# Optimization experiments

Hardware: AMD Instinct MI355X
Metric: run time of the kernel (lower is better)

The kernel has to match this reference:

```python
import jax, jax.numpy as jnp
import numpy as np

G = 4
EPS = 1e-5

def group_norm(x, gamma, beta):
    B, C, D, H, W = x.shape
    xg = x.reshape(B, G, C // G, D, H, W)
    mu = xg.mean(axis=(2, 3, 4, 5), keepdims=True)
    var = xg.var(axis=(2, 3, 4, 5), keepdims=True)
    xn = ((xg - mu) * jax.lax.rsqrt(var + EPS)).reshape(B, C, D, H, W)
    return xn * gamma[None, :, None, None, None] + beta[None, :, None, None, None]

def conv3d(x, w, b):
    y = jax.lax.conv_general_dilated(x, w, (1, 1, 1), [(1, 1), (1, 1), (1, 1)],
                                     dimension_numbers=('NCDHW', 'OIDHW', 'NCDHW'))
    return y + b[None, :, None, None, None]

def deform_conv_hw(x, offset, w, b):
    # x: [B,C,D,H,W]; offset: [B, 2*27, D,H,W] -> per-tap (dh, dw); depth taps are rigid.
    B, C, D, H, W = x.shape
    off = offset.reshape(B, 27, 2, D, H, W)
    xp = jnp.pad(x, ((0, 0), (0, 0), (1, 1), (0, 0), (0, 0)))  # zero-pad depth only
    hh = jnp.arange(H, dtype=x.dtype)[None, None, :, None]
    ww = jnp.arange(W, dtype=x.dtype)[None, None, None, :]
    bi = jnp.arange(B)[:, None, None, None]
    di = jnp.arange(D)[None, :, None, None]
    out = jnp.zeros((B, w.shape[0], D, H, W), x.dtype)
    tap = 0
    for i in range(3):
        x_d = xp[:, :, i:i + D]  # depth-shifted view [B,C,D,H,W]
        for j in range(3):
            for k in range(3):
                hp = hh + (j - 1) + off[:, tap, 0]  # [B,D,H,W] fractional h position
                wp = ww + (k - 1) + off[:, tap, 1]
                h0 = jnp.floor(hp); w0 = jnp.floor(wp)
                h0i = h0.astype(jnp.int32); w0i = w0.astype(jnp.int32)
                lh = hp - h0; lw = wp - w0
                def gather(hi, wi):
                    m = ((hi >= 0) & (hi < H) & (wi >= 0) & (wi < W)).astype(x.dtype)
                    g = x_d[bi, :, di, jnp.clip(hi, 0, H - 1), jnp.clip(wi, 0, W - 1)]  # [B,D,H,W,C]
                    return g, m
                g00, m00 = gather(h0i, w0i)
                g01, m01 = gather(h0i, w0i + 1)
                g10, m10 = gather(h0i + 1, w0i)
                g11, m11 = gather(h0i + 1, w0i + 1)
                val = (((1 - lh) * (1 - lw) * m00)[..., None] * g00
                       + ((1 - lh) * lw * m01)[..., None] * g01
                       + (lh * (1 - lw) * m10)[..., None] * g10
                       + (lh * lw * m11)[..., None] * g11)
                out = out + jnp.einsum('bdhwc,oc->bodhw', val, w[:, :, i, j, k])
                tap += 1
    return out + b[None, :, None, None, None]

def setup_inputs():
    key = jax.random.key(0)
    ks = jax.random.split(key, 8)
    B, C, D, H, W = 1, 32, 24, 96, 96
    x = jax.random.normal(ks[0], (B, C, D, H, W), jnp.float32)
    g1 = jnp.ones((C,), jnp.float32); be1 = jnp.zeros((C,), jnp.float32)
    g2 = jnp.ones((C,), jnp.float32); be2 = jnp.zeros((C,), jnp.float32)
    ow1 = jax.random.normal(ks[1], (54, C, 3, 3, 3), jnp.float32) * 0.02
    ob1 = jnp.zeros((54,), jnp.float32)
    dw1 = jax.random.normal(ks[2], (C, C, 3, 3, 3), jnp.float32) * 0.05
    db1 = jnp.zeros((C,), jnp.float32)
    ow2 = jax.random.normal(ks[3], (54, C, 3, 3, 3), jnp.float32) * 0.02
    ob2 = jnp.zeros((54,), jnp.float32)
    dw2 = jax.random.normal(ks[4], (C, C, 3, 3, 3), jnp.float32) * 0.05
    db2 = jnp.zeros((C,), jnp.float32)
    return {"x": x, "g1": g1, "be1": be1, "g2": g2, "be2": be2,
            "ow1": ow1, "ob1": ob1, "dw1": dw1, "db1": db1,
            "ow2": ow2, "ob2": ob2, "dw2": dw2, "db2": db2}

def reference(x, g1, be1, g2, be2, ow1, ob1, dw1, db1, ow2, ob2, dw2, db2):
    h = jax.nn.relu(group_norm(x, g1, be1))
    h = deform_conv_hw(h, conv3d(h, ow1, ob1), dw1, db1)
    h = jax.nn.relu(group_norm(h, g2, be2))
    h = deform_conv_hw(h, conv3d(h, ow2, ob2), dw2, db2)
    return h + x
```

## Files before the change

### kernel.cpp

```cpp
#include <hip/hip_runtime.h>
#include <hip/hip_fp16.h>

#define CC   32
#define DD   24
#define HH   96
#define WW   96
#define HWC  (HH*WW)
#define DHW  (DD*HH*WW)
#define NG   4
#define CPG  (CC/NG)
#define OC1  54
#define GN_EPS 1e-5f

#define NBLK_F (DHW/128)
#define CHUNK_F (NBLK_F/8)
#define NBLK_G (DHW/256)
#define CHUNK_G (NBLK_G/8)

typedef float  f32x4 __attribute__((ext_vector_type(4)));
typedef _Float16 f16x8 __attribute__((ext_vector_type(8)));
typedef unsigned int u32x4 __attribute__((ext_vector_type(4)));

union F16Frag { f16x8 v; __half2 h2[4]; };

__device__ __forceinline__ int swz(int bid, int chunk) {
    return (bid % 8) * chunk + (bid / 8);
}

__global__ void pack_w(const float* __restrict__ src, _Float16* __restrict__ dst,
                       int O, int NT, int n) {
    int idx = blockIdx.x * 256 + threadIdx.x;
    if (idx >= n) return;
    int e    = idx & 7;
    int lane = (idx >> 3) & 63;
    int nt   = (idx >> 9) % NT;
    int tap  = (idx >> 9) / NT;
    int o = nt * 16 + (lane & 15);
    int c = (lane >> 4) * 8 + e;
    float v = (o < O) ? src[(o * CC + c) * 27 + tap] : 0.f;
    dst[idx] = (_Float16)v;
}

__global__ void gn_stats(const float* __restrict__ x, float* __restrict__ stats) {
    const int g = blockIdx.x >> 5;
    const int s = blockIdx.x & 31;
    const float4* base = (const float4*)(x + (size_t)g * CPG * DHW);
    const int n4 = CPG * DHW / 4;
    float s1 = 0.f, s2 = 0.f;
    for (int idx = s * 256 + threadIdx.x; idx < n4; idx += 32 * 256) {
        float4 v = base[idx];
        s1 += v.x + v.y + v.z + v.w;
        s2 += v.x * v.x + v.y * v.y + v.z * v.z + v.w * v.w;
    }
    for (int off = 32; off > 0; off >>= 1) {
        s1 += __shfl_down(s1, off);
        s2 += __shfl_down(s2, off);
    }
    __shared__ float ls1[4], ls2[4];
    int wid = threadIdx.x >> 6;
    if ((threadIdx.x & 63) == 0) { ls1[wid] = s1; ls2[wid] = s2; }
    __syncthreads();
    if (threadIdx.x == 0) {
        float a = 0.f, b = 0.f;
        for (int i = 0; i < 4; i++) { a += ls1[i]; b += ls2[i]; }
        atomicAdd(&stats[g * 2 + 0], a);
        atomicAdd(&stats[g * 2 + 1], b);
    }
}

__global__ void gn_apply_T(const float* __restrict__ x, const float* __restrict__ stats,
                           const float* __restrict__ gamma, const float* __restrict__ beta,
                           __half* __restrict__ yT) {
    const int p = swz(blockIdx.x, CHUNK_G) * 256 + threadIdx.x;
    const float invN = 1.0f / (float)(CPG * DHW);
    float mean[NG], rstd[NG];
#pragma unroll
    for (int g = 0; g < NG; g++) {
        mean[g] = stats[2 * g] * invN;
        float var = stats[2 * g + 1] * invN - mean[g] * mean[g];
        rstd[g] = rsqrtf(var + GN_EPS);
    }
    float vals[CC];
#pragma unroll
    for (int c = 0; c < CC; c++) {
        const int g = c >> 3;
        const float ga = gamma[c] * rstd[g];
        const float be = beta[c] - mean[g] * ga;
        vals[c] = fmaxf(0.f, x[(size_t)c * DHW + p] * ga + be);
    }
    union { __half2 h2[16]; u32x4 q[4]; } u;
#pragma unroll
    for (int c = 0; c < 16; c++) u.h2[c] = __floats2half2_rn(vals[2 * c], vals[2 * c + 1]);
    u32x4* dst = (u32x4*)(yT + (size_t)p * CC);
#pragma unroll
    for (int q = 0; q < 4; q++) dst[q] = u.q[q];
}

__global__ __launch_bounds__(128, 3) void fused_conv(const __half* __restrict__ xT,
                                                     const _Float16* __restrict__ wBo,
                                                     const float* __restrict__ ob,
                                                     const _Float16* __restrict__ wBd,
                                                     const float* __restrict__ db,
                                                     const float* __restrict__ resid,
                                                     float* __restrict__ outp) {
    __shared__ __align__(16) char lds_raw[CC * 132 * 4];
    __half* offs_lds = (__half*)lds_raw;
    float*  out_lds  = (float*)lds_raw;

    const int tid  = threadIdx.x;
    const int lane = tid & 63;
    const int wave = tid >> 6;
    const int p0   = swz(blockIdx.x, CHUNK_F) * 128;
    const int pw   = p0 + wave * 64;
    const int d    = pw / HWC;
    const int rem  = pw % HWC;
    const int mrow = lane & 15;
    const int kg   = lane >> 4;
    const int wbase2 = wave * (27 * 64 * 2);

    int hq[4], wq[4];
#pragma unroll
    for (int m = 0; m < 4; m++) {
        int rr = rem + m * 16 + mrow;
        hq[m] = rr / WW; wq[m] = rr % WW;
    }

    f32x4 aco[4][4];
#pragma unroll
    for (int m = 0; m < 4; m++)
#pragma unroll
        for (int n = 0; n < 4; n++) aco[m][n] = (f32x4){0.f, 0.f, 0.f, 0.f};

    const f16x8* wbo8 = (const f16x8*)wBo;

#pragma unroll 1
    for (int i = 0; i < 3; i++) {
        const int dd = d + i - 1;
        if ((unsigned)dd >= DD) continue;
        const __half* xd = xT + (size_t)dd * HWC * CC;
#pragma unroll 3
        for (int jk = 0; jk < 9; jk++) {
            const int j = jk / 3, k = jk % 3, tap = i * 9 + jk;
            const f16x8 b0 = wbo8[(tap * 4 + 0) * 64 + lane];
            const f16x8 b1 = wbo8[(tap * 4 + 1) * 64 + lane];
            const f16x8 b2 = wbo8[(tap * 4 + 2) * 64 + lane];
            const f16x8 b3 = wbo8[(tap * 4 + 3) * 64 + lane];
            f16x8 a[4];
#pragma unroll
            for (int m = 0; m < 4; m++) {
                const int hh = hq[m] + j - 1;
                const int ww = wq[m] + k - 1;
                a[m] = (f16x8){0, 0, 0, 0, 0, 0, 0, 0};
                if ((unsigned)hh < HH && (unsigned)ww < WW)
                    a[m] = *(const f16x8*)(xd + (size_t)(hh * WW + ww) * CC + kg * 8);
            }
#pragma unroll
            for (int m = 0; m < 4; m++) {
                aco[m][0] = __builtin_amdgcn_mfma_f32_16x16x32_f16(a[m], b0, aco[m][0], 0, 0, 0);
                aco[m][1] = __builtin_amdgcn_mfma_f32_16x16x32_f16(a[m], b1, aco[m][1], 0, 0, 0);
                aco[m][2] = __builtin_amdgcn_mfma_f32_16x16x32_f16(a[m], b2, aco[m][2], 0, 0, 0);
                aco[m][3] = __builtin_amdgcn_mfma_f32_16x16x32_f16(a[m], b3, aco[m][3], 0, 0, 0);
            }
        }
    }

    float bo[4];
#pragma unroll
    for (int nt = 0; nt < 4; nt++) {
        const int o = nt * 16 + mrow;
        bo[nt] = (o < OC1) ? ob[o] : 0.f;
    }
#pragma unroll
    for (int m = 0; m < 4; m++) {
#pragma unroll
        for (int nt = 0; nt < 4; nt++) {
            const int o = nt * 16 + mrow;
            if (o < OC1) {
                const int tap = o >> 1, par = o & 1;
#pragma unroll
                for (int r = 0; r < 4; r++) {
                    const int pt = m * 16 + kg * 4 + r;
                    offs_lds[wbase2 + tap * 128 + pt * 2 + par] =
                        __float2half(aco[m][nt][r] + bo[nt]);
                }
            }
        }
    }
    __syncthreads();

    f32x4 acd[4][2];
#pragma unroll
    for (int m = 0; m < 4; m++) {
        acd[m][0] = (f32x4){0.f, 0.f, 0.f, 0.f};
        acd[m][1] = (f32x4){0.f, 0.f, 0.f, 0.f};
    }

    const f16x8* wbd8 = (const f16x8*)wBd;

#pragma unroll 1
    for (int i = 0; i < 3; i++) {
        const int dd = d + i - 1;
        if ((unsigned)dd >= DD) continue;
        const __half* xd = xT + (size_t)dd * HWC * CC;
        unsigned int offn[4];
#pragma unroll
        for (int m = 0; m < 4; m++)
            offn[m] = *(const unsigned int*)&offs_lds[wbase2 + (i * 9) * 128 + (m * 16 + mrow) * 2];
#pragma unroll 1
        for (int jk = 0; jk < 9; jk++) {
            const int j = jk / 3, k = jk % 3, tap = i * 9 + jk;
            const f16x8 b0 = wbd8[(tap * 2 + 0) * 64 + lane];
            const f16x8 b1 = wbd8[(tap * 2 + 1) * 64 + lane];
            unsigned int offc[4];
#pragma unroll
            for (int m = 0; m < 4; m++) offc[m] = offn[m];
            if (jk < 8) {
#pragma unroll
                for (int m = 0; m < 4; m++)
                    offn[m] = *(const unsigned int*)&offs_lds[wbase2 + (tap + 1) * 128 + (m * 16 + mrow) * 2];
            }
            int i00[4], i01[4], i10[4], i11[4];
            float c00[4], c01[4], c10[4], c11[4];
#pragma unroll
            for (int m = 0; m < 4; m++) {
                const __half2 o2 = *(__half2*)&offc[m];
                const float oh = __half2float(__low2half(o2));
                const float ov = __half2float(__high2half(o2));
                const float hp  = (float)(hq[m] + j - 1) + oh;
                const float wpf = (float)(wq[m] + k - 1) + ov;
                const float h0f = floorf(hp), w0f = floorf(wpf);
                const int h0 = (int)h0f, w0 = (int)w0f;
                const float lh = hp - h0f, lw = wpf - w0f;
                const bool hv0 = (h0 >= 0) && (h0 < HH);
                const bool hv1 = (h0 >= -1) && (h0 < HH - 1);
                const bool wv0 = (w0 >= 0) && (w0 < WW);
                const bool wv1 = (w0 >= -1) && (w0 < WW - 1);
                c00[m] = (hv0 && wv0) ? (1.f - lh) * (1.f - lw) : 0.f;
                c01[m] = (hv0 && wv1) ? (1.f - lh) * lw : 0.f;
                c10[m] = (hv1 && wv0) ? lh * (1.f - lw) : 0.f;
                c11[m] = (hv1 && wv1) ? lh * lw : 0.f;
                const int h0c = min(max(h0, 0), HH - 1);
                const int h1c = min(max(h0 + 1, 0), HH - 1);
                const int w0c = min(max(w0, 0), WW - 1);
                const int w1c = min(max(w0 + 1, 0), WW - 1);
                i00[m] = h0c * WW + w0c;
                i01[m] = h0c * WW + w1c;
                i10[m] = h1c * WW + w0c;
                i11[m] = h1c * WW + w1c;
            }
#pragma unroll
            for (int m = 0; m < 4; m++) {
                F16Frag a00, a01, a10, a11, A;
                a00.v = *(const f16x8*)(xd + (size_t)i00[m] * CC + kg * 8);
                a01.v = *(const f16x8*)(xd + (size_t)i01[m] * CC + kg * 8);
                a10.v = *(const f16x8*)(xd + (size_t)i10[m] * CC + kg * 8);
                a11.v = *(const f16x8*)(xd + (size_t)i11[m] * CC + kg * 8);
                const __half2 C00 = __float2half2_rn(c00[m]);
                const __half2 C01 = __float2half2_rn(c01[m]);
                const __half2 C10 = __float2half2_rn(c10[m]);
                const __half2 C11 = __float2half2_rn(c11[m]);
#pragma unroll
                for (int r = 0; r < 4; r++) {
                    __half2 t = __hmul2(C00, a00.h2[r]);
                    t = __hfma2(C01, a01.h2[r], t);
                    t = __hfma2(C10, a10.h2[r], t);
                    t = __hfma2(C11, a11.h2[r], t);
                    A.h2[r] = t;
                }
                acd[m][0] = __builtin_amdgcn_mfma_f32_16x16x32_f16(A.v, b0, acd[m][0], 0, 0, 0);
                acd[m][1] = __builtin_amdgcn_mfma_f32_16x16x32_f16(A.v, b1, acd[m][1], 0, 0, 0);
            }
        }
    }
    __syncthreads();

#pragma unroll
    for (int m = 0; m < 4; m++)
#pragma unroll
        for (int nt = 0; nt < 2; nt++) {
            const int o = nt * 16 + mrow;
            *(f32x4*)&out_lds[o * 132 + wave * 64 + m * 16 + kg * 4] = acd[m][nt];
        }
    __syncthreads();
    if (resid) {
#pragma unroll 1
        for (int o = 0; o < CC; o++) {
            float v = out_lds[o * 132 + tid] + db[o] + resid[(size_t)o * DHW + p0 + tid];
            outp[(size_t)o * DHW + p0 + tid] = v;
        }
    } else {
#pragma unroll 1
        for (int o = 0; o < CC; o++)
            outp[(size_t)o * DHW + p0 + tid] = out_lds[o * 132 + tid] + db[o];
    }
}

extern "C" void kernel_launch(void* const* d_in, const int* in_sizes, int n_in,
                              void* d_out, int out_size, void* d_ws, size_t ws_size,
                              hipStream_t stream) {
    const float* x   = (const float*)d_in[0];
    const float* g1  = (const float*)d_in[1];
    const float* be1 = (const float*)d_in[2];
    const float* g2  = (const float*)d_in[3];
    const float* be2 = (const float*)d_in[4];
    const float* ow1 = (const float*)d_in[5];
    const float* ob1 = (const float*)d_in[6];
    const float* dw1 = (const float*)d_in[7];
    const float* db1 = (const float*)d_in[8];
    const float* ow2 = (const float*)d_in[9];
    const float* ob2 = (const float*)d_in[10];
    const float* dw2 = (const float*)d_in[11];
    const float* db2 = (const float*)d_in[12];
    float* out = (float*)d_out;
    float* ws  = (float*)d_ws;

    float*    stats = ws;
    _Float16* wBo1  = (_Float16*)(ws + 256);
    _Float16* wBd1  = (_Float16*)(ws + 27904);
    _Float16* wBo2  = (_Float16*)(ws + 41728);
    _Float16* wBd2  = (_Float16*)(ws + 69376);
    __half*   hT    = (__half*)(ws + 83200);

    (void)hipMemsetAsync(stats, 0, 16 * sizeof(float), stream);
    pack_w<<<(27 * 4 * 512 + 255) / 256, 256, 0, stream>>>(ow1, wBo1, 54, 4, 27 * 4 * 512);
    pack_w<<<(27 * 2 * 512 + 255) / 256, 256, 0, stream>>>(dw1, wBd1, 32, 2, 27 * 2 * 512);
    pack_w<<<(27 * 4 * 512 + 255) / 256, 256, 0, stream>>>(ow2, wBo2, 54, 4, 27 * 4 * 512);
    pack_w<<<(27 * 2 * 512 + 255) / 256, 256, 0, stream>>>(dw2, wBd2, 32, 2, 27 * 2 * 512);

    gn_stats<<<NG * 32, 256, 0, stream>>>(x, stats + 0);
    gn_apply_T<<<NBLK_G, 256, 0, stream>>>(x, stats + 0, g1, be1, hT);
    fused_conv<<<NBLK_F, 128, 0, stream>>>(hT, wBo1, ob1, wBd1, db1, nullptr, out);

    gn_stats<<<NG * 32, 256, 0, stream>>>(out, stats + 8);
    gn_apply_T<<<NBLK_G, 256, 0, stream>>>(out, stats + 8, g2, be2, hT);
    fused_conv<<<NBLK_F, 128, 0, stream>>>(hT, wBo2, ob2, wBd2, db2, x, out);
}
```

Measured before the change: 368.2 us.

## Stage halo input rows into LDS for the offset convolution

For each depth tap, the block cooperatively loads four padded input rows (the block's rows plus a one-row halo) into shared memory, using a padded channel stride. The nine h/w taps then read their MFMA A fragments from LDS instead of issuing repeated global loads. This trades redundant global and cache traffic for two barriers per depth slice and a larger LDS footprint, which may limit occupancy.

```diff
diff --git a/kernel.cpp b/kernel.cpp
--- a/kernel.cpp
+++ b/kernel.cpp
@@ -16,6 +16,9 @@
 #define CHUNK_F (NBLK_F/8)
 #define NBLK_G (DHW/256)
 #define CHUNK_G (NBLK_G/8)
+
+#define XS_STRIDE 40
+#define XS_PTS    (4*WW)
 
 typedef float  f32x4 __attribute__((ext_vector_type(4)));
 typedef _Float16 f16x8 __attribute__((ext_vector_type(8)));
@@ -103,7 +106,8 @@
                                                      const float* __restrict__ db,
                                                      const float* __restrict__ resid,
                                                      float* __restrict__ outp) {
-    __shared__ __align__(16) char lds_raw[CC * 132 * 4];
+    __shared__ __align__(16) char lds_raw[XS_PTS * XS_STRIDE * 2];
+    __half* xs       = (__half*)lds_raw;
     __half* offs_lds = (__half*)lds_raw;
     float*  out_lds  = (float*)lds_raw;
 
@@ -112,7 +116,8 @@
     const int wave = tid >> 6;
     const int p0   = swz(blockIdx.x, CHUNK_F) * 128;
     const int pw   = p0 + wave * 64;
-    const int d    = pw / HWC;
+    const int d    = p0 / HWC;
+    const int r0   = (p0 % HWC) / WW;
     const int rem  = pw % HWC;
     const int mrow = lane & 15;
     const int kg   = lane >> 4;
@@ -137,7 +142,23 @@
     for (int i = 0; i < 3; i++) {
         const int dd = d + i - 1;
         if ((unsigned)dd >= DD) continue;
-        const __half* xd = xT + (size_t)dd * HWC * CC;
+        const __half* xsrc = xT + (size_t)dd * HWC * CC;
+
+        __syncthreads();
+#pragma unroll
+        for (int rd = 0; rd < 12; rd++) {
+            const int fi  = rd * 128 + tid;
+            const int pt  = fi >> 2;
+            const int q   = fi & 3;
+            const int row = r0 - 1 + (pt / WW);
+            const int wc  = pt % WW;
+            f16x8 v = {0, 0, 0, 0, 0, 0, 0, 0};
+            if ((unsigned)row < HH)
+                v = *(const f16x8*)(xsrc + ((size_t)row * WW + wc) * CC + q * 8);
+            *(f16x8*)(xs + pt * XS_STRIDE + q * 8) = v;
+        }
+        __syncthreads();
+
 #pragma unroll 3
         for (int jk = 0; jk < 9; jk++) {
             const int j = jk / 3, k = jk % 3, tap = i * 9 + jk;
@@ -148,11 +169,11 @@
             f16x8 a[4];
 #pragma unroll
             for (int m = 0; m < 4; m++) {
-                const int hh = hq[m] + j - 1;
+                const int lr = hq[m] + j - r0;
                 const int ww = wq[m] + k - 1;
                 a[m] = (f16x8){0, 0, 0, 0, 0, 0, 0, 0};
-                if ((unsigned)hh < HH && (unsigned)ww < WW)
-                    a[m] = *(const f16x8*)(xd + (size_t)(hh * WW + ww) * CC + kg * 8);
+                if ((unsigned)ww < WW)
+                    a[m] = *(const f16x8*)(xs + (size_t)(lr * WW + ww) * XS_STRIDE + kg * 8);
             }
 #pragma unroll
             for (int m = 0; m < 4; m++) {
@@ -163,6 +184,7 @@
             }
         }
     }
+    __syncthreads();
 
     float bo[4];
 #pragma unroll
```

After: 389.7 us. +5.8%, slower.

## Fuse second GroupNorm statistics into first conv epilogue and merge weight packing

Applied to the files above, without the earlier changes.

The first fused_conv now accumulates per-group sum and sum-of-squares of its output in the store loop, reduces them across each wave with shuffles, and adds them to global stats with atomics. This removes the separate gn_stats pass that re-read the whole intermediate tensor. The four pack_w launches and the memset are merged into one pack_all kernel to cut launch overhead. In exchange, fp32 atomic accumulation order becomes nondeterministic, and the conv epilogue carries extra register pressure and about 2k atomics per group.

```diff
diff --git a/kernel.cpp b/kernel.cpp
--- a/kernel.cpp
+++ b/kernel.cpp
@@ -27,18 +27,29 @@
     return (bid % 8) * chunk + (bid / 8);
 }
 
-__global__ void pack_w(const float* __restrict__ src, _Float16* __restrict__ dst,
-                       int O, int NT, int n) {
+__global__ void pack_all(const float* __restrict__ ow1, const float* __restrict__ dw1,
+                         const float* __restrict__ ow2, const float* __restrict__ dw2,
+                         _Float16* __restrict__ wBo1, _Float16* __restrict__ wBd1,
+                         _Float16* __restrict__ wBo2, _Float16* __restrict__ wBd2,
+                         float* __restrict__ stats) {
     int idx = blockIdx.x * 256 + threadIdx.x;
-    if (idx >= n) return;
-    int e    = idx & 7;
-    int lane = (idx >> 3) & 63;
-    int nt   = (idx >> 9) % NT;
-    int tap  = (idx >> 9) / NT;
+    if (blockIdx.x == 0 && threadIdx.x < 16) stats[threadIdx.x] = 0.f;
+    const int NO = 27 * 4 * 512;
+    const int ND = 27 * 2 * 512;
+    const float* src; _Float16* dst; int O, NT, rel;
+    if (idx < NO)                       { src = ow1; dst = wBo1; O = 54; NT = 4; rel = idx; }
+    else if (idx < NO + ND)             { src = dw1; dst = wBd1; O = 32; NT = 2; rel = idx - NO; }
+    else if (idx < 2 * NO + ND)         { src = ow2; dst = wBo2; O = 54; NT = 4; rel = idx - NO - ND; }
+    else if (idx < 2 * NO + 2 * ND)     { src = dw2; dst = wBd2; O = 32; NT = 2; rel = idx - 2 * NO - ND; }
+    else return;
+    int e    = rel & 7;
+    int lane = (rel >> 3) & 63;
+    int nt   = (rel >> 9) % NT;
+    int tap  = (rel >> 9) / NT;
     int o = nt * 16 + (lane & 15);
     int c = (lane >> 4) * 8 + e;
     float v = (o < O) ? src[(o * CC + c) * 27 + tap] : 0.f;
-    dst[idx] = (_Float16)v;
+    dst[rel] = (_Float16)v;
 }
 
 __global__ void gn_stats(const float* __restrict__ x, float* __restrict__ stats) {
@@ -102,7 +113,8 @@
                                                      const _Float16* __restrict__ wBd,
                                                      const float* __restrict__ db,
                                                      const float* __restrict__ resid,
-                                                     float* __restrict__ outp) {
+                                                     float* __restrict__ outp,
+                                                     float* __restrict__ stats_out) {
     __shared__ __align__(16) char lds_raw[CC * 132 * 4];
     __half* offs_lds = (__half*)lds_raw;
     float*  out_lds  = (float*)lds_raw;
@@ -289,9 +301,31 @@
             outp[(size_t)o * DHW + p0 + tid] = v;
         }
     } else {
-#pragma unroll 1
-        for (int o = 0; o < CC; o++)
-            outp[(size_t)o * DHW + p0 + tid] = out_lds[o * 132 + tid] + db[o];
+        float s1l[NG] = {0.f, 0.f, 0.f, 0.f};
+        float s2l[NG] = {0.f, 0.f, 0.f, 0.f};
+#pragma unroll 1
+        for (int o = 0; o < CC; o++) {
+            float v = out_lds[o * 132 + tid] + db[o];
+            outp[(size_t)o * DHW + p0 + tid] = v;
+            s1l[o >> 3] += v;
+            s2l[o >> 3] += v * v;
+        }
+        if (stats_out) {
+            for (int off = 32; off > 0; off >>= 1) {
+#pragma unroll
+                for (int g = 0; g < NG; g++) {
+                    s1l[g] += __shfl_down(s1l[g], off);
+                    s2l[g] += __shfl_down(s2l[g], off);
+                }
+            }
+            if (lane == 0) {
+#pragma unroll
+                for (int g = 0; g < NG; g++) {
+                    atomicAdd(&stats_out[2 * g + 0], s1l[g]);
+                    atomicAdd(&stats_out[2 * g + 1], s2l[g]);
+                }
+            }
+        }
     }
 }
 
@@ -321,17 +355,13 @@
     _Float16* wBd2  = (_Float16*)(ws + 69376);
     __half*   hT    = (__half*)(ws + 83200);
 
-    (void)hipMemsetAsync(stats, 0, 16 * sizeof(float), stream);
-    pack_w<<<(27 * 4 * 512 + 255) / 256, 256, 0, stream>>>(ow1, wBo1, 54, 4, 27 * 4 * 512);
-    pack_w<<<(27 * 2 * 512 + 255) / 256, 256, 0, stream>>>(dw1, wBd1, 32, 2, 27 * 2 * 512);
-    pack_w<<<(27 * 4 * 512 + 255) / 256, 256, 0, stream>>>(ow2, wBo2, 54, 4, 27 * 4 * 512);
-    pack_w<<<(27 * 2 * 512 + 255) / 256, 256, 0, stream>>>(dw2, wBd2, 32, 2, 27 * 2 * 512);
+    pack_all<<<(2 * 55296 + 2 * 27648 + 255) / 256, 256, 0, stream>>>(
+        ow1, dw1, ow2, dw2, wBo1, wBd1, wBo2, wBd2, stats);
 
     gn_stats<<<NG * 32, 256, 0, stream>>>(x, stats + 0);
     gn_apply_T<<<NBLK_G, 256, 0, stream>>>(x, stats + 0, g1, be1, hT);
-    fused_conv<<<NBLK_F, 128, 0, stream>>>(hT, wBo1, ob1, wBd1, db1, nullptr, out);
-
-    gn_stats<<<NG * 32, 256, 0, stream>>>(out, stats + 8);
+    fused_conv<<<NBLK_F, 128, 0, stream>>>(hT, wBo1, ob1, wBd1, db1, nullptr, out, stats + 8);
+
     gn_apply_T<<<NBLK_G, 256, 0, stream>>>(out, stats + 8, g2, be2, hT);
-    fused_conv<<<NBLK_F, 128, 0, stream>>>(hT, wBo2, ob2, wBd2, db2, x, out);
-}
+    fused_conv<<<NBLK_F, 128, 0, stream>>>(hT, wBo2, ob2, wBd2, db2, x, out, nullptr);
+}
```

Result: slower. 640.6 us (+74.0%).
